# Performance work log

Hardware: AMD Instinct MI355X
Metric: run time of the kernel (lower is better)

Reference implementation:

```python
import jax, jax.numpy as jnp
import numpy as np

E, H, LQ, LC, B = 1024, 16, 1024, 512, 4
HD = E // H
FF = 4 * E
EPS = 1e-6


def _rope(x):
    # x: [B, H, L, D]; interleaved rotary embedding (lucidrains-style)
    D, L = x.shape[-1], x.shape[-2]
    inv_freq = 1.0 / (10000.0 ** (jnp.arange(0, D, 2, dtype=jnp.float32) / D))
    ang = jnp.arange(L, dtype=jnp.float32)[:, None] * inv_freq[None, :]  # [L, D/2]
    cos, sin = jnp.cos(ang), jnp.sin(ang)
    x1, x2 = x[..., 0::2], x[..., 1::2]
    r1 = x1 * cos - x2 * sin
    r2 = x1 * sin + x2 * cos
    return jnp.stack([r1, r2], axis=-1).reshape(x.shape)


def _ln(x, w, b):
    mu = jnp.mean(x, -1, keepdims=True)
    var = jnp.mean(jnp.square(x - mu), -1, keepdims=True)
    return (x - mu) * jax.lax.rsqrt(var + EPS) * w + b


def _rope_attn(x, ctx, qw, qb, kw, kb, vw, vb, pw, pb, mask):
    Bn, L, Em = x.shape
    Lc = ctx.shape[1]
    q = (x @ qw.T + qb).reshape(Bn, L, H, HD).transpose(0, 2, 1, 3)
    k = (ctx @ kw.T + kb).reshape(Bn, Lc, H, HD).transpose(0, 2, 1, 3)
    v = (ctx @ vw.T + vb).reshape(Bn, Lc, H, HD).transpose(0, 2, 1, 3)
    q, k = _rope(q), _rope(k)
    s = jnp.einsum('bhic,bhjc->bhij', q, k) / np.sqrt(HD).astype(np.float32)
    if mask is not None:
        s = jnp.where(mask[None, None], -jnp.inf, s)
    p = jax.nn.softmax(s, axis=-1)
    o = jnp.einsum('bhij,bhjc->bhic', p, v)
    o = o.transpose(0, 2, 1, 3).reshape(Bn, L, Em)
    return o @ pw.T + pb


def setup_inputs() -> dict:
    key = jax.random.key(0)
    ks = iter(jax.random.split(key, 40))
    s = 0.02
    d = {}
    d['x'] = jax.random.normal(next(ks), (B, LQ, E), jnp.float32)
    d['context'] = jax.random.normal(next(ks), (B, LC, E), jnp.float32)
    d['attn_mask'] = jnp.triu(jnp.ones((LQ, LQ), bool), k=1)  # True = masked (causal)
    for g in ('g_msa', 'g_ca', 'g_mlp'):
        d[g] = jax.random.normal(next(ks), (1, 1, E), jnp.float32) * s
    for n in ('n1', 'n2', 'n3'):
        d[n + '_w'] = jnp.ones((E,), jnp.float32)
        d[n + '_b'] = jnp.zeros((E,), jnp.float32)
    for p in ('sa', 'ca'):
        for m in ('q', 'k', 'v', 'p'):
            d[f'{p}_{m}w'] = jax.random.normal(next(ks), (E, E), jnp.float32) * s
            d[f'{p}_{m}b'] = jnp.zeros((E,), jnp.float32)
    d['fc1_w'] = jax.random.normal(next(ks), (FF, E), jnp.float32) * s
    d['fc1_b'] = jnp.zeros((FF,), jnp.float32)
    d['fc2_w'] = jax.random.normal(next(ks), (E, FF), jnp.float32) * s
    d['fc2_b'] = jnp.zeros((E,), jnp.float32)
    return d


def reference(x, context, attn_mask,
              g_msa, g_ca, g_mlp,
              n1_w, n1_b, n2_w, n2_b, n3_w, n3_b,
              sa_qw, sa_qb, sa_kw, sa_kb, sa_vw, sa_vb, sa_pw, sa_pb,
              ca_qw, ca_qb, ca_kw, ca_kb, ca_vw, ca_vb, ca_pw, ca_pb,
              fc1_w, fc1_b, fc2_w, fc2_b):
    # self-attention (causal RoPE) with zero-init learned gate
    x = x + g_msa * _rope_attn(_ln(x, n1_w, n1_b), _ln(x, n1_w, n1_b),
                               sa_qw, sa_qb, sa_kw, sa_kb, sa_vw, sa_vb,
                               sa_pw, sa_pb, attn_mask)
    # cross-attention (RoPE on both streams, no mask)
    h = _ln(x, n2_w, n2_b)
    x = x + g_ca * _rope_attn(h, context,
                              ca_qw, ca_qb, ca_kw, ca_kb, ca_vw, ca_vb,
                              ca_pw, ca_pb, None)
    # gated MLP with tanh-approx GELU
    h = _ln(x, n3_w, n3_b)
    h = jax.nn.gelu(h @ fc1_w.T + fc1_b, approximate=True) @ fc2_w.T + fc2_b
    x = x + g_mlp * h
    return x
```

## Files before the change

kernel.cpp:

```cpp
#include <hip/hip_runtime.h>
#include <math.h>

#if !__has_builtin(__builtin_amdgcn_cvt_pk_fp8_f32)
#include <hip/hip_fp8.h>
#endif

typedef __attribute__((ext_vector_type(8))) short short8;
typedef __attribute__((ext_vector_type(4))) float f32x4;
typedef __attribute__((ext_vector_type(16))) float f32x16;
typedef unsigned char u8;
typedef unsigned short u16;
typedef unsigned int u32;
typedef __attribute__((ext_vector_type(2))) u32 u32x2;
typedef __attribute__((ext_vector_type(4))) u32 u32x4;
typedef __attribute__((ext_vector_type(8))) int i32x8;
typedef unsigned long long u64;

static constexpr int E = 1024, H = 16, LQ = 1024, LC = 512, Bn = 4, FF = 4096;
static constexpr int NTOK = Bn * LQ;
static constexpr int NCTX = Bn * LC;

#define QSCALE 0.1803368801111244f
#define DEFER_THR 11.5f

static constexpr size_t OFF_TCOS   = 0;
static constexpr size_t OFF_TSIN   = OFF_TCOS + (size_t)LQ*32*4;
static constexpr size_t OFF_BSAQKV = OFF_TSIN + (size_t)LQ*32*4;
static constexpr size_t OFF_BCAKV  = OFF_BSAQKV + 16384;
static constexpr size_t OFF_WSAQKV = OFF_BCAKV + 16384;
static constexpr size_t OFF_WSAP   = OFF_WSAQKV + (size_t)3072*1024*2;
static constexpr size_t OFF_WCAQ   = OFF_WSAP   + (size_t)1024*1024*2;
static constexpr size_t OFF_WCAKV  = OFF_WCAQ   + (size_t)1024*1024*2;
static constexpr size_t OFF_WCAP   = OFF_WCAKV  + (size_t)2048*1024*2;
static constexpr size_t OFF_WFC1   = OFF_WCAP   + (size_t)1024*1024*2;
static constexpr size_t OFF_WFC2   = OFF_WFC1   + (size_t)4096*1024*2;
static constexpr size_t OFF_CTXB   = OFF_WFC2   + (size_t)1024*4096*2;
static constexpr size_t OFF_H      = OFF_CTXB   + (size_t)2048*1024*2;
static constexpr size_t OFF_QKV    = OFF_H      + (size_t)4096*1024*2;
static constexpr size_t OFF_CAQ    = OFF_QKV;
static constexpr size_t OFF_CAKV   = OFF_QKV + (size_t)4096*1024*2;
static constexpr size_t OFF_QR     = OFF_QKV + (size_t)4096*3072*2;
static constexpr size_t OFF_KR     = OFF_QR  + (size_t)4096*1024*2;
static constexpr size_t OFF_VT     = OFF_KR  + (size_t)4096*1024*2;
static constexpr size_t OFF_AO     = OFF_VT  + (size_t)4096*1024*2;
static constexpr size_t OFF_U      = OFF_QKV;
static constexpr size_t WS_NEED    = OFF_AO + (size_t)4096*1024*2;

static constexpr size_t OFF_W8QKV = OFF_WFC1;
static constexpr size_t OFF_W8FC1 = OFF_W8QKV + (size_t)3072*1024;
static constexpr size_t OFF_W8FC2 = OFF_W8FC1 + (size_t)4096*1024;

static __device__ __forceinline__ float bf2f(u16 u) {
  union { u32 i; float f; } un; un.i = ((u32)u) << 16; return un.f;
}
static __device__ __forceinline__ u16 f2bf(float f) {
  union { float f; u32 u; } un; un.f = f;
  u32 u = un.u;
  return (u16)((u + 0x7FFFu + ((u >> 16) & 1u)) >> 16);
}
static __device__ __forceinline__ u64 pack4(u16 a, u16 b, u16 c, u16 d) {
  return (u64)a | ((u64)b << 16) | ((u64)c << 32) | ((u64)d << 48);
}
static __device__ __forceinline__ f32x4 mfma16(short8 a, short8 b, f32x4 c) {
  return __builtin_amdgcn_mfma_f32_16x16x32_bf16(a, b, c, 0, 0, 0);
}
static __device__ __forceinline__ f32x16 mfma32(short8 a, short8 b, f32x16 c) {
  return __builtin_amdgcn_mfma_f32_32x32x16_bf16(a, b, c, 0, 0, 0);
}
static __device__ __forceinline__ void gload_lds16(void* lds, const void* g) {
  __builtin_amdgcn_global_load_lds(
      (const __attribute__((address_space(1))) void*)g,
      (__attribute__((address_space(3))) void*)lds, 16, 0, 0);
}
static __device__ __forceinline__ float gelu_tanh(float x) {
  float z2 = 1.5957691216057308f * (x + 0.044715f * x * x * x);
  float e = __expf(z2);
  float r = __builtin_amdgcn_rcpf(e + 1.0f);
  return x - x * r;
}
static __device__ __forceinline__ u32 cvtpk_bf16(float lo, float hi) {
  u32 r;
  asm("v_cvt_pk_bf16_f32 %0, %1, %2" : "=v"(r) : "v"(lo), "v"(hi));
  return r;
}
static __device__ __forceinline__ u32 pack_fp8x4(float a, float b, float c, float d) {
#if __has_builtin(__builtin_amdgcn_cvt_pk_fp8_f32)
  u32 r = (u32)__builtin_amdgcn_cvt_pk_fp8_f32(a, b, 0, false);
  r = (u32)__builtin_amdgcn_cvt_pk_fp8_f32(c, d, (int)r, true);
  return r;
#else
  __hip_fp8_e4m3 qa(a), qb(b), qc(c), qd(d);
  return (u32)qa.__x | ((u32)qb.__x << 8) | ((u32)qc.__x << 16) | ((u32)qd.__x << 24);
#endif
}
static __device__ __forceinline__ u8 fp8b(float f) {
#if __has_builtin(__builtin_amdgcn_cvt_pk_fp8_f32)
  return (u8)((u32)__builtin_amdgcn_cvt_pk_fp8_f32(f, f, 0, false) & 0xFFu);
#else
  __hip_fp8_e4m3 t(f); return t.__x;
#endif
}

__global__ __launch_bounds__(256) void build_tab(float* __restrict__ ct, float* __restrict__ st) {
  int idx = blockIdx.x * 256 + threadIdx.x;
  int pos = idx >> 5, i = idx & 31;
  float inv = powf(10000.f, -(float)i * (1.f / 32.f));
  float a = (float)pos * inv;
  ct[idx] = cosf(a);
  st[idx] = sinf(a);
}

struct Cvt11 { const float* s[11]; };
__global__ __launch_bounds__(256) void cvt_all(Cvt11 a, u16* __restrict__ dst) {
  u32 gid = blockIdx.x * 256 + threadIdx.x;
  u32 s, off;
  if (gid < 2097152u)      { s = gid >> 18; if (s < 3) return;     off = gid & 262143u; }
  else if (gid < 4194304u) { return; }
  else                     { s = 10;                               off = gid - 4194304u; }
  float4 v = *(const float4*)(a.s[s] + (size_t)off * 4);
  *(u64*)(dst + (size_t)gid * 4) = pack4(f2bf(v.x), f2bf(v.y), f2bf(v.z), f2bf(v.w));
}

__global__ __launch_bounds__(256) void cvt_fp8b(const float* __restrict__ qw, const float* __restrict__ kw,
                                                const float* __restrict__ vw, const float* __restrict__ f1,
                                                const float* __restrict__ f2,
                                                u8* __restrict__ d_qkv, u8* __restrict__ d_f1,
                                                u8* __restrict__ d_f2) {
  u32 gid = blockIdx.x * 256 + threadIdx.x;
  u32 seg = gid >> 18, off = gid & 262143u;
  const float* s; u8* d;
  if (seg < 3)      { s = seg == 0 ? qw : (seg == 1 ? kw : vw); d = d_qkv + (size_t)seg * 1048576; }
  else if (seg < 7) { s = f1 + (size_t)(seg - 3) * 1048576;     d = d_f1  + (size_t)(seg - 3) * 1048576; }
  else              { s = f2 + (size_t)(seg - 7) * 1048576;     d = d_f2  + (size_t)(seg - 7) * 1048576; }
  float4 v = *(const float4*)(s + (size_t)off * 4);
  *(u32*)(d + (size_t)off * 4) =
      pack_fp8x4(v.x * 256.f, v.y * 256.f, v.z * 256.f, v.w * 256.f);
}

struct Cp5 { const float* s[5]; };
__global__ __launch_bounds__(256) void copy5(Cp5 a, float* __restrict__ dst) {
  int gid = blockIdx.x * 256 + threadIdx.x;
  int s = gid >> 10, off = gid & 1023;
  int doff = (s < 3) ? s * 1024 : 4096 + (s - 3) * 1024;
  dst[doff + off] = a.s[s][off];
}

__global__ __launch_bounds__(256) void init_bias_gate(float* __restrict__ out, const float* __restrict__ bias,
                                                      const float* __restrict__ gate) {
  int i = (blockIdx.x * 256 + threadIdx.x) * 4;
  int c = i & 1023;
  float4 o = *(float4*)(out + i);
  o.x += gate[c] * bias[c];
  o.y += gate[c + 1] * bias[c + 1];
  o.z += gate[c + 2] * bias[c + 2];
  o.w += gate[c + 3] * bias[c + 3];
  *(float4*)(out + i) = o;
}

__global__ __launch_bounds__(256) void ln_bf16(const float* __restrict__ x, const float* __restrict__ w,
                                               const float* __restrict__ b, u16* __restrict__ out) {
  __shared__ float red[4];
  int row = blockIdx.x, tid = threadIdx.x;
  const float* xr = x + (size_t)row * 1024;
  float4 v = ((const float4*)xr)[tid];
  float s = v.x + v.y + v.z + v.w;
#pragma unroll
  for (int off = 32; off; off >>= 1) s += __shfl_xor(s, off);
  if ((tid & 63) == 0) red[tid >> 6] = s;
  __syncthreads();
  float mean = (red[0] + red[1] + red[2] + red[3]) * (1.f / 1024.f);
  float dx = v.x - mean, dy = v.y - mean, dz = v.z - mean, dw = v.w - mean;
  float sq = dx * dx + dy * dy + dz * dz + dw * dw;
#pragma unroll
  for (int off = 32; off; off >>= 1) sq += __shfl_xor(sq, off);
  __syncthreads();
  if ((tid & 63) == 0) red[tid >> 6] = sq;
  __syncthreads();
  float var = (red[0] + red[1] + red[2] + red[3]) * (1.f / 1024.f);
  float rstd = rsqrtf(var + 1e-6f);
  float4 wv = ((const float4*)w)[tid];
  float4 bv = ((const float4*)b)[tid];
  u64 o = pack4(f2bf(dx * rstd * wv.x + bv.x), f2bf(dy * rstd * wv.y + bv.y),
                f2bf(dz * rstd * wv.z + bv.z), f2bf(dw * rstd * wv.w + bv.w));
  *(u64*)(out + (size_t)row * 1024 + tid * 4) = o;
}

__global__ __launch_bounds__(256) void ln_fp8(const float* __restrict__ x, const float* __restrict__ w,
                                              const float* __restrict__ b, u8* __restrict__ out) {
  __shared__ float red[4];
  int row = blockIdx.x, tid = threadIdx.x;
  const float* xr = x + (size_t)row * 1024;
  float4 v = ((const float4*)xr)[tid];
  float s = v.x + v.y + v.z + v.w;
#pragma unroll
  for (int off = 32; off; off >>= 1) s += __shfl_xor(s, off);
  if ((tid & 63) == 0) red[tid >> 6] = s;
  __syncthreads();
  float mean = (red[0] + red[1] + red[2] + red[3]) * (1.f / 1024.f);
  float dx = v.x - mean, dy = v.y - mean, dz = v.z - mean, dw = v.w - mean;
  float sq = dx * dx + dy * dy + dz * dz + dw * dw;
#pragma unroll
  for (int off = 32; off; off >>= 1) sq += __shfl_xor(sq, off);
  __syncthreads();
  if ((tid & 63) == 0) red[tid >> 6] = sq;
  __syncthreads();
  float var = (red[0] + red[1] + red[2] + red[3]) * (1.f / 1024.f);
  float rstd = rsqrtf(var + 1e-6f);
  float4 wv = ((const float4*)w)[tid];
  float4 bv = ((const float4*)b)[tid];
  u32 pk = pack_fp8x4((dx * rstd * wv.x + bv.x) * 16.f, (dy * rstd * wv.y + bv.y) * 16.f,
                      (dz * rstd * wv.z + bv.z) * 16.f, (dw * rstd * wv.w + bv.w) * 16.f);
  *(u32*)(out + (size_t)row * 1024 + tid * 4) = pk;
}

struct RopeJob { const u16* src; u16* dst; int ld, col0, Lper, T; float scale; };
struct Rope2 { RopeJob j[2]; };
__global__ __launch_bounds__(128) void rope2(Rope2 a, const float* __restrict__ cosT,
                                             const float* __restrict__ sinT) {
  RopeJob jb = a.j[blockIdx.y];
  int t = blockIdx.x;
  if (t >= jb.T) return;
  int b = t / jb.Lper, l = t - b * jb.Lper;
  int tid = threadIdx.x;
  int e0 = tid * 8;
  int h = e0 >> 6, d0 = e0 & 63;
  short8 vv = *(const short8*)(jb.src + (size_t)t * jb.ld + jb.col0 + e0);
  short8 ov;
#pragma unroll
  for (int j = 0; j < 4; ++j) {
    float x1 = bf2f((u16)vv[2 * j]);
    float x2 = bf2f((u16)vv[2 * j + 1]);
    int i = (d0 >> 1) + j;
    float c = cosT[l * 32 + i], s = sinT[l * 32 + i];
    ov[2 * j]     = (short)f2bf((x1 * c - x2 * s) * jb.scale);
    ov[2 * j + 1] = (short)f2bf((x1 * s + x2 * c) * jb.scale);
  }
  *(short8*)(jb.dst + (((size_t)b * H + h) * jb.Lper + l) * 64 + d0) = ov;
}

__global__ __launch_bounds__(256) void vtrans(const u16* __restrict__ src, int ld, int col0,
                                              u16* __restrict__ dst, int Lper) {
  __shared__ u16 tile[64][72];
  int bh = blockIdx.y;
  int b = bh >> 4, h = bh & 15;
  int l0 = blockIdx.x * 64;
  int tid = threadIdx.x;
#pragma unroll
  for (int j = 0; j < 2; ++j) {
    int c = tid + j * 256;
    int i = c >> 3, d0 = (c & 7) * 8;
    short8 v = *(const short8*)(src + (size_t)(b * Lper + l0 + i) * ld + col0 + h * 64 + d0);
    *(short8*)(&tile[i][d0]) = v;
  }
  __syncthreads();
#pragma unroll
  for (int j = 0; j < 2; ++j) {
    int c = tid + j * 256;
    int d = c >> 3, lc = (c & 7) * 8;
    short8 v;
#pragma unroll
    for (int k = 0; k < 8; ++k) v[k] = (short)tile[lc + k][d];
    *(short8*)(dst + (((size_t)bh) * 64 + d) * Lper + l0 + lc) = v;
  }
}

enum { EPI_BF16 = 0, EPI_GELU = 1, EPI_RESID = 2 };

template <int EPI>
__global__ __launch_bounds__(512, 4) void gemm2(const u16* __restrict__ A, const u16* __restrict__ W,
                                                const float* __restrict__ bias, u16* outb, float* outf,
                                                const float* res, const float* __restrict__ gate,
                                                int M, int N, int K) {
  __shared__ u16 As[2][128 * 64];
  __shared__ u16 Bs[2][128 * 64];

  int nwg = gridDim.x * gridDim.y;
  int bid = blockIdx.y * gridDim.x + blockIdx.x;
  int cpx = nwg >> 3;
  int swz = (bid & 7) * cpx + (bid >> 3);
  int bx = swz % gridDim.x;
  int by = swz / gridDim.x;
  int row0 = by * 128, col0 = bx * 128;

  int tid = threadIdx.x;
  int lane = tid & 63, wid = tid >> 6;
  int wr = wid >> 2, wc = wid & 3;
  int lr = lane & 15, lg = lane >> 4;

  size_t a_off0, a_off1, b_off0, b_off1;
  int l_off0 = tid * 8, l_off1 = (512 + tid) * 8;
  {
    int q = tid, r = q >> 3, p = q & 7, sp = p ^ (r & 7);
    a_off0 = (size_t)(row0 + r) * K + sp * 8;
    b_off0 = (size_t)(col0 + r) * K + sp * 8;
    q = 512 + tid; r = q >> 3; p = q & 7; sp = p ^ (r & 7);
    a_off1 = (size_t)(row0 + r) * K + sp * 8;
    b_off1 = (size_t)(col0 + r) * K + sp * 8;
  }

  f32x4 acc[4][2] = {};

  const int nkt = K >> 6;
  {
    gload_lds16(&As[0][l_off0], A + a_off0);
    gload_lds16(&Bs[0][l_off0], W + b_off0);
    gload_lds16(&As[0][l_off1], A + a_off1);
    gload_lds16(&Bs[0][l_off1], W + b_off1);
  }
  __syncthreads();

  for (int kt = 0; kt < nkt; ++kt) {
    int cur = kt & 1;
    if (kt + 1 < nkt) {
      int k0 = (kt + 1) << 6;
      gload_lds16(&As[cur ^ 1][l_off0], A + a_off0 + k0);
      gload_lds16(&Bs[cur ^ 1][l_off0], W + b_off0 + k0);
      gload_lds16(&As[cur ^ 1][l_off1], A + a_off1 + k0);
      gload_lds16(&Bs[cur ^ 1][l_off1], W + b_off1 + k0);
    }
#pragma unroll
    for (int kk = 0; kk < 2; ++kk) {
      short8 af[4], bfr[2];
#pragma unroll
      for (int m = 0; m < 4; ++m) {
        int r = wr * 64 + m * 16 + lr;
        int sc = (kk * 4 + lg) ^ (r & 7);
        af[m] = *(const short8*)(&As[cur][r * 64 + sc * 8]);
      }
#pragma unroll
      for (int n = 0; n < 2; ++n) {
        int r = wc * 32 + n * 16 + lr;
        int sc = (kk * 4 + lg) ^ (r & 7);
        bfr[n] = *(const short8*)(&Bs[cur][r * 64 + sc * 8]);
      }
#pragma unroll
      for (int m = 0; m < 4; ++m)
#pragma unroll
        for (int n = 0; n < 2; ++n)
          acc[m][n] = mfma16(af[m], bfr[n], acc[m][n]);
    }
    __syncthreads();
  }

  if (EPI == EPI_BF16 || EPI == EPI_GELU) {
    u16* Ct = &As[0][0];
#pragma unroll
    for (int n = 0; n < 2; ++n) {
      int c = wc * 32 + n * 16 + lr;
      float bv = bias[col0 + c];
#pragma unroll
      for (int m = 0; m < 4; ++m) {
#pragma unroll
        for (int i = 0; i < 4; ++i) {
          int r = wr * 64 + m * 16 + lg * 4 + i;
          float v = acc[m][n][i] + bv;
          Ct[r * 128 + c] = f2bf(EPI == EPI_GELU ? gelu_tanh(v) : v);
        }
      }
    }
    __syncthreads();
#pragma unroll
    for (int j = 0; j < 4; ++j) {
      u32 q = (u32)tid + j * 512;
      u32 r = q >> 4, ck = q & 15;
      short8 v = *(const short8*)(Ct + r * 128 + ck * 8);
      *(short8*)(outb + (size_t)(row0 + r) * N + col0 + ck * 8) = v;
    }
  } else {
#pragma unroll
    for (int n = 0; n < 2; ++n) {
      int cg = col0 + wc * 32 + n * 16 + lr;
      float bv = bias[cg];
#pragma unroll
      for (int m = 0; m < 4; ++m) {
#pragma unroll
        for (int i = 0; i < 4; ++i) {
          int rg = row0 + wr * 64 + m * 16 + lg * 4 + i;
          float v = acc[m][n][i] + bv;
          float r = res[(size_t)rg * N + cg];
          outf[(size_t)rg * N + cg] = r + gate[cg] * v;
        }
      }
    }
  }
}

enum { E8_BF16 = 0, E8_GELU = 1, E8_ATOMIC = 2 };

template <int EPI>
__global__ __launch_bounds__(256, 2) void gemm8(const u8* __restrict__ A, const u8* __restrict__ W,
                                                const float* __restrict__ bias, u16* outb16,
                                                u8* outb8, float* outf, const float* __restrict__ gate,
                                                int M, int N, int K, int kchunks) {
  __shared__ u8 As[2][128 * 128];
  __shared__ u8 Bs[2][128 * 128];

  int nwg = gridDim.x * gridDim.y;
  int bid = blockIdx.y * gridDim.x + blockIdx.x;
  int cpx = nwg >> 3;
  int swz = (bid & 7) * cpx + (bid >> 3);
  int bx = swz % gridDim.x, by = swz / gridDim.x;
  int row0 = by * 128, col0 = bx * 128;

  const int Kc = K / kchunks;
  const int kbase = blockIdx.z * Kc;

  int tid = threadIdx.x;
  int lane = tid & 63, wid = tid >> 6;
  int wr = wid >> 1, wc = wid & 1;
  int lr = lane & 15, lg = lane >> 4;

  u32 aoff[4], boff[4];
  int ldso[4];
#pragma unroll
  for (int j = 0; j < 4; ++j) {
    int q = tid + j * 256;
    int r = q >> 3, p = q & 7, sp = p ^ (r & 7);
    aoff[j] = (u32)(row0 + r) * (u32)K + sp * 16;
    boff[j] = (u32)(col0 + r) * (u32)K + sp * 16;
    ldso[j] = q * 16;
  }

  f32x4 acc[4][4] = {};
  const int nkt = Kc >> 7;

  auto rdfrag = [&](const u8* base, int r, i32x8& f) {
    const u8* rp = base + r * 128;
    int ck = lg * 2;
    u32x4 lo = *(const u32x4*)(rp + ((ck) ^ (r & 7)) * 16);
    u32x4 hh = *(const u32x4*)(rp + ((ck + 1) ^ (r & 7)) * 16);
    i32x8 v;
    v[0] = (int)lo[0]; v[1] = (int)lo[1]; v[2] = (int)lo[2]; v[3] = (int)lo[3];
    v[4] = (int)hh[0]; v[5] = (int)hh[1]; v[6] = (int)hh[2]; v[7] = (int)hh[3];
    f = v;
  };

#pragma unroll
  for (int j = 0; j < 4; ++j) {
    gload_lds16(&As[0][ldso[j]], A + aoff[j] + kbase);
    gload_lds16(&Bs[0][ldso[j]], W + boff[j] + kbase);
  }
  __syncthreads();

  for (int kt = 0; kt < nkt; ++kt) {
    int cur = kt & 1;
    if (kt + 1 < nkt) {
      int k0 = kbase + ((kt + 1) << 7);
#pragma unroll
      for (int j = 0; j < 4; ++j) {
        gload_lds16(&As[cur ^ 1][ldso[j]], A + aoff[j] + k0);
        gload_lds16(&Bs[cur ^ 1][ldso[j]], W + boff[j] + k0);
      }
    }
    i32x8 a[4], b[4];
#pragma unroll
    for (int m = 0; m < 4; ++m) rdfrag(&As[cur][0], wr * 64 + m * 16 + lr, a[m]);
#pragma unroll
    for (int n = 0; n < 4; ++n) rdfrag(&Bs[cur][0], wc * 64 + n * 16 + lr, b[n]);
    __builtin_amdgcn_s_setprio(1);
#pragma unroll
    for (int m = 0; m < 4; ++m)
#pragma unroll
      for (int n = 0; n < 4; ++n)
        acc[m][n] = __builtin_amdgcn_mfma_scale_f32_16x16x128_f8f6f4(
            a[m], b[n], acc[m][n], 0, 0, 0, 0x7F7F7F7F, 0, 0x7F7F7F7F);
    __builtin_amdgcn_s_setprio(0);
    __syncthreads();
  }

  constexpr float SCL = 1.f / 4096.f;
  if (EPI == E8_BF16) {
    u16* Ct = (u16*)&As[0][0];
#pragma unroll
    for (int n = 0; n < 4; ++n) {
      int cl = wc * 64 + n * 16 + lr;
      float bv = bias[col0 + cl];
#pragma unroll
      for (int m = 0; m < 4; ++m) {
#pragma unroll
        for (int i = 0; i < 4; ++i) {
          int rl = wr * 64 + m * 16 + lg * 4 + i;
          Ct[rl * 128 + cl] = f2bf(acc[m][n][i] * SCL + bv);
        }
      }
    }
    __syncthreads();
#pragma unroll
    for (int j = 0; j < 8; ++j) {
      u32 q = (u32)tid + j * 256;
      u32 r = q >> 4, ck = q & 15;
      short8 v = *(const short8*)(Ct + r * 128 + ck * 8);
      *(short8*)(outb16 + (size_t)(row0 + r) * N + col0 + ck * 8) = v;
    }
  } else if (EPI == E8_GELU) {
    u8* Ct = &As[0][0];
#pragma unroll
    for (int n = 0; n < 4; ++n) {
      int cl = wc * 64 + n * 16 + lr;
      float bv = bias[col0 + cl];
#pragma unroll
      for (int m = 0; m < 4; ++m) {
#pragma unroll
        for (int i = 0; i < 4; ++i) {
          int rl = wr * 64 + m * 16 + lg * 4 + i;
          float v = acc[m][n][i] * SCL + bv;
          Ct[rl * 128 + cl] = fp8b(gelu_tanh(v) * 16.f);
        }
      }
    }
    __syncthreads();
#pragma unroll
    for (int j = 0; j < 4; ++j) {
      int q = tid + j * 256;
      int r = q >> 3, ck = q & 7;
      *(u32x4*)(outb8 + (size_t)(row0 + r) * N + col0 + ck * 16) =
          *(const u32x4*)(Ct + r * 128 + ck * 16);
    }
  } else {
#pragma unroll
    for (int n = 0; n < 4; ++n) {
      int cg = col0 + wc * 64 + n * 16 + lr;
      float gv = gate[cg];
#pragma unroll
      for (int m = 0; m < 4; ++m) {
#pragma unroll
        for (int i = 0; i < 4; ++i) {
          int rg = row0 + wr * 64 + m * 16 + lg * 4 + i;
          atomicAdd(&outf[(size_t)rg * N + cg], gv * (acc[m][n][i] * SCL));
        }
      }
    }
  }
}

template <int MASKED, int PRE>
static __device__ __forceinline__ void attn_tile3(short8* kf, const u16* KtNext,
                                                  const u16* Vp0, const u16* Vp1,
                                                  const short8* qf, int kb, int q0, int l31, int hi,
                                                  float& m, float& lsum, f32x16& o0, f32x16& o1) {
  short8 vf0[4], vf1[4];
#pragma unroll
  for (int ks = 0; ks < 4; ++ks) {
    vf0[ks] = *(const short8*)(Vp0 + ks * 16 + hi * 8);
    vf1[ks] = *(const short8*)(Vp1 + ks * 16 + hi * 8);
  }
  f32x16 s0 = {}, s1 = {};
  __builtin_amdgcn_s_setprio(1);
#pragma unroll
  for (int s = 0; s < 4; ++s) {
    s0 = mfma32(kf[s], qf[s], s0);
    s1 = mfma32(kf[4 + s], qf[s], s1);
  }
  __builtin_amdgcn_s_setprio(0);
  if (PRE) {
    const u16* kp0 = KtNext + (size_t)l31 * 64 + hi * 8;
    const u16* kp1 = KtNext + (size_t)(32 + l31) * 64 + hi * 8;
#pragma unroll
    for (int s = 0; s < 4; ++s) {
      kf[s] = *(const short8*)(kp0 + s * 16);
      kf[4 + s] = *(const short8*)(kp1 + s * 16);
    }
  }
  if (MASKED) {
    int qg = q0 + l31;
#pragma unroll
    for (int r = 0; r < 16; ++r) {
      int kk = kb + (r & 3) + 8 * (r >> 2) + 4 * hi;
      if (kk > qg) s0[r] = -INFINITY;
      if (kk + 32 > qg) s1[r] = -INFINITY;
    }
  }
  float pm = -INFINITY;
#pragma unroll
  for (int r = 0; r < 16; ++r) pm = fmaxf(pm, fmaxf(s0[r], s1[r]));
  pm = fmaxf(pm, __shfl_xor(pm, 32));
  if (!__all(pm <= m + DEFER_THR)) {
    float mn = fmaxf(m, pm);
    float al = exp2f(m - mn);
    m = mn;
    lsum *= al;
#pragma unroll
    for (int r = 0; r < 16; ++r) {
      float alr = __shfl(al, (r & 3) + 8 * (r >> 2) + 4 * hi);
      o0[r] *= alr;
      o1[r] *= alr;
    }
  }
  float ts = 0.f;
#pragma unroll
  for (int r = 0; r < 16; ++r) {
    float p0 = exp2f(s0[r] - m);
    float p1 = exp2f(s1[r] - m);
    s0[r] = p0; s1[r] = p1;
    ts += p0 + p1;
  }
  ts += __shfl_xor(ts, 32);
  lsum += ts;
  auto pack8 = [&](float a0, float a1, float a2, float a3,
                   float a4, float a5, float a6, float a7) -> short8 {
    u32 c0 = cvtpk_bf16(a0, a1), c1 = cvtpk_bf16(a2, a3);
    u32 c2 = cvtpk_bf16(a4, a5), c3 = cvtpk_bf16(a6, a7);
    u32x2 r02 = __builtin_amdgcn_permlane32_swap(c0, c2, false, false);
    u32x2 r13 = __builtin_amdgcn_permlane32_swap(c1, c3, false, false);
    u32x4 w;
    w[0] = r02[0]; w[1] = r13[0]; w[2] = r02[1]; w[3] = r13[1];
    return __builtin_bit_cast(short8, w);
  };
  short8 pa0 = pack8(s0[0], s0[1], s0[2], s0[3], s0[4], s0[5], s0[6], s0[7]);
  short8 pa1 = pack8(s0[8], s0[9], s0[10], s0[11], s0[12], s0[13], s0[14], s0[15]);
  short8 pa2 = pack8(s1[0], s1[1], s1[2], s1[3], s1[4], s1[5], s1[6], s1[7]);
  short8 pa3 = pack8(s1[8], s1[9], s1[10], s1[11], s1[12], s1[13], s1[14], s1[15]);
  short8 pa[4] = {pa0, pa1, pa2, pa3};
  __builtin_amdgcn_s_setprio(1);
#pragma unroll
  for (int ks = 0; ks < 4; ++ks) {
    o0 = mfma32(pa[ks], vf0[ks], o0);
    o1 = mfma32(pa[ks], vf1[ks], o1);
  }
  __builtin_amdgcn_s_setprio(0);
}

template <int CAUSAL>
__global__ __launch_bounds__(256) void flash_attn2(const u16* __restrict__ Q, const u16* __restrict__ K,
                                                   const u16* __restrict__ Vt, u16* __restrict__ O,
                                                   int Lq, int Lk) {
  const int wid = threadIdx.x >> 6, lane = threadIdx.x & 63;
  const int l31 = lane & 31, hi = lane >> 5;
  int wg = blockIdx.x * 4 + wid;
  int bh = wg & 63;
  int qc = wg >> 6;
  if (CAUSAL) qc = (Lq >> 5) - 1 - qc;
  int q0 = qc << 5;

  const u16* Qb = Q + ((size_t)bh * Lq + q0) * 64;
  const u16* Kb = K + (size_t)bh * Lk * 64;
  const u16* Vb = Vt + (size_t)bh * 64 * Lk;

  short8 qf[4];
#pragma unroll
  for (int s = 0; s < 4; ++s) qf[s] = *(const short8*)(Qb + (size_t)l31 * 64 + s * 16 + hi * 8);

  f32x16 o0 = {}, o1 = {};
  float m = -INFINITY, lsum = 0.f;

  const u16* Kt = Kb;
  const u16* Vp0 = Vb + (size_t)l31 * Lk;
  const u16* Vp1 = Vb + (size_t)(32 + l31) * Lk;

  short8 kf[8];
  {
    const u16* kp0 = Kt + (size_t)l31 * 64 + hi * 8;
    const u16* kp1 = Kt + (size_t)(32 + l31) * 64 + hi * 8;
#pragma unroll
    for (int s = 0; s < 4; ++s) {
      kf[s] = *(const short8*)(kp0 + s * 16);
      kf[4 + s] = *(const short8*)(kp1 + s * 16);
    }
  }

  int nt = CAUSAL ? ((q0 >> 6) + 1) : (Lk >> 6);
  for (int t = 0; t < nt - 1; ++t) {
    attn_tile3<0, 1>(kf, Kt + 64 * 64, Vp0, Vp1, qf, t * 64, q0, l31, hi, m, lsum, o0, o1);
    Kt += 64 * 64; Vp0 += 64; Vp1 += 64;
  }
  if (CAUSAL)
    attn_tile3<1, 0>(kf, nullptr, Vp0, Vp1, qf, (nt - 1) * 64, q0, l31, hi, m, lsum, o0, o1);
  else
    attn_tile3<0, 0>(kf, nullptr, Vp0, Vp1, qf, (nt - 1) * 64, q0, l31, hi, m, lsum, o0, o1);

  float myinv = 1.f / lsum;
  int b = bh >> 4, h = bh & 15;
#pragma unroll
  for (int r = 0; r < 16; ++r) {
    int cr = (r & 3) + 8 * (r >> 2) + 4 * hi;
    float li = __shfl(myinv, cr);
    u16* op = O + ((size_t)b * Lq + q0 + cr) * 1024 + h * 64;
    op[l31] = f2bf(o0[r] * li);
    op[32 + l31] = f2bf(o1[r] * li);
  }
}

extern "C" void kernel_launch(void* const* d_in, const int* in_sizes, int n_in,
                              void* d_out, int out_size, void* d_ws, size_t ws_size,
                              hipStream_t stream) {
  (void)in_sizes; (void)n_in; (void)out_size;
  if (ws_size < WS_NEED) return;

  const float* x     = (const float*)d_in[0];
  const float* ctx   = (const float*)d_in[1];
  const float* g_msa = (const float*)d_in[3];
  const float* g_ca  = (const float*)d_in[4];
  const float* g_mlp = (const float*)d_in[5];
  const float* n1w = (const float*)d_in[6],  *n1b = (const float*)d_in[7];
  const float* n2w = (const float*)d_in[8],  *n2b = (const float*)d_in[9];
  const float* n3w = (const float*)d_in[10], *n3b = (const float*)d_in[11];
  const float* sa_qw = (const float*)d_in[12], *sa_kw = (const float*)d_in[14];
  const float* sa_vw = (const float*)d_in[16], *sa_pw = (const float*)d_in[18];
  const float* sa_qb = (const float*)d_in[13], *sa_kb = (const float*)d_in[15];
  const float* sa_vb = (const float*)d_in[17], *sa_pb = (const float*)d_in[19];
  const float* ca_qw = (const float*)d_in[20], *ca_qb = (const float*)d_in[21];
  const float* ca_kw = (const float*)d_in[22], *ca_kb = (const float*)d_in[23];
  const float* ca_vw = (const float*)d_in[24], *ca_vb = (const float*)d_in[25];
  const float* ca_pw = (const float*)d_in[26], *ca_pb = (const float*)d_in[27];
  const float* fc1w = (const float*)d_in[28], *fc1b = (const float*)d_in[29];
  const float* fc2w = (const float*)d_in[30], *fc2b = (const float*)d_in[31];

  char* ws = (char*)d_ws;
  float* out = (float*)d_out;
  float* tcos = (float*)(ws + OFF_TCOS);
  float* tsin = (float*)(ws + OFF_TSIN);
  u16* Hb   = (u16*)(ws + OFF_H);
  u16* QKV  = (u16*)(ws + OFF_QKV);
  u16* QR   = (u16*)(ws + OFF_QR);
  u16* KR   = (u16*)(ws + OFF_KR);
  u16* VT   = (u16*)(ws + OFF_VT);
  u16* AO   = (u16*)(ws + OFF_AO);
  u8*  H8   = (u8*)(ws + OFF_H);
  u8*  U8   = (u8*)(ws + OFF_U);
  u8*  W8QKV = (u8*)(ws + OFF_W8QKV);
  u8*  W8FC1 = (u8*)(ws + OFF_W8FC1);
  u8*  W8FC2 = (u8*)(ws + OFF_W8FC2);

  build_tab<<<dim3(128), dim3(256), 0, stream>>>(tcos, tsin);

  Cvt11 ca;
  ca.s[0] = sa_qw; ca.s[1] = sa_kw; ca.s[2] = sa_vw; ca.s[3] = sa_pw;
  ca.s[4] = ca_qw; ca.s[5] = ca_kw; ca.s[6] = ca_vw; ca.s[7] = ca_pw;
  ca.s[8] = fc1w;  ca.s[9] = fc2w;  ca.s[10] = ctx;
  cvt_all<<<dim3(18432), dim3(256), 0, stream>>>(ca, (u16*)(ws + OFF_WSAQKV));
  cvt_fp8b<<<dim3(11264), dim3(256), 0, stream>>>(sa_qw, sa_kw, sa_vw, fc1w, fc2w,
                                                  W8QKV, W8FC1, W8FC2);
  Cp5 cp;
  cp.s[0] = sa_qb; cp.s[1] = sa_kb; cp.s[2] = sa_vb; cp.s[3] = ca_kb; cp.s[4] = ca_vb;
  copy5<<<dim3(20), dim3(256), 0, stream>>>(cp, (float*)(ws + OFF_BSAQKV));

  ln_fp8<<<dim3(NTOK), dim3(256), 0, stream>>>(x, n1w, n1b, H8);
  gemm8<E8_BF16><<<dim3(3072 / 128, NTOK / 128), dim3(256), 0, stream>>>(
      H8, W8QKV, (float*)(ws + OFF_BSAQKV), QKV, nullptr, nullptr, nullptr,
      NTOK, 3072, 1024, 1);
  {
    Rope2 r;
    r.j[0] = {QKV, QR, 3072, 0,    LQ, NTOK, QSCALE};
    r.j[1] = {QKV, KR, 3072, 1024, LQ, NTOK, 1.0f};
    rope2<<<dim3(NTOK, 2), dim3(128), 0, stream>>>(r, tcos, tsin);
  }
  vtrans<<<dim3(LQ / 64, Bn * H), dim3(256), 0, stream>>>(QKV, 3072, 2048, VT, LQ);
  flash_attn2<1><<<dim3(512), dim3(256), 0, stream>>>(QR, KR, VT, AO, LQ, LQ);
  gemm2<EPI_RESID><<<dim3(1024 / 128, NTOK / 128), dim3(512), 0, stream>>>(
      AO, (u16*)(ws + OFF_WSAP), sa_pb, nullptr, out, x, g_msa, NTOK, 1024, 1024);

  ln_bf16<<<dim3(NTOK), dim3(256), 0, stream>>>(out, n2w, n2b, Hb);
  gemm2<EPI_BF16><<<dim3(1024 / 128, NTOK / 128), dim3(512), 0, stream>>>(
      Hb, (u16*)(ws + OFF_WCAQ), ca_qb, (u16*)(ws + OFF_CAQ), nullptr, nullptr, nullptr,
      NTOK, 1024, 1024);
  gemm2<EPI_BF16><<<dim3(2048 / 128, NCTX / 128), dim3(512), 0, stream>>>(
      (u16*)(ws + OFF_CTXB), (u16*)(ws + OFF_WCAKV), (float*)(ws + OFF_BCAKV),
      (u16*)(ws + OFF_CAKV), nullptr, nullptr, nullptr, NCTX, 2048, 1024);
  {
    Rope2 r;
    r.j[0] = {(u16*)(ws + OFF_CAQ),  QR, 1024, 0, LQ, NTOK, QSCALE};
    r.j[1] = {(u16*)(ws + OFF_CAKV), KR, 2048, 0, LC, NCTX, 1.0f};
    rope2<<<dim3(NTOK, 2), dim3(128), 0, stream>>>(r, tcos, tsin);
  }
  vtrans<<<dim3(LC / 64, Bn * H), dim3(256), 0, stream>>>(
      (u16*)(ws + OFF_CAKV), 2048, 1024, VT, LC);
  flash_attn2<0><<<dim3(512), dim3(256), 0, stream>>>(QR, KR, VT, AO, LQ, LC);
  gemm2<EPI_RESID><<<dim3(1024 / 128, NTOK / 128), dim3(512), 0, stream>>>(
      AO, (u16*)(ws + OFF_WCAP), ca_pb, nullptr, out, out, g_ca, NTOK, 1024, 1024);

  ln_fp8<<<dim3(NTOK), dim3(256), 0, stream>>>(out, n3w, n3b, H8);
  gemm8<E8_GELU><<<dim3(4096 / 128, NTOK / 128), dim3(256), 0, stream>>>(
      H8, W8FC1, fc1b, nullptr, U8, nullptr, nullptr, NTOK, 4096, 1024, 1);
  init_bias_gate<<<dim3(4096), dim3(256), 0, stream>>>(out, fc2b, g_mlp);
  gemm8<E8_ATOMIC><<<dim3(1024 / 128, NTOK / 128, 2), dim3(256), 0, stream>>>(
      U8, W8FC2, nullptr, nullptr, nullptr, out, g_mlp, NTOK, 1024, 4096, 2);
}
```

Before: 326.7 us.

## Move projection and cross-attention GEMMs to FP8 and emit attention output in FP8

Four GEMMs switch from the bf16 gemm2 path to the FP8 gemm8 path: self-attention output projection, cross-attention Q, cross-attention KV and cross-attention output projection. gemm8 gains a new residual/gate epilogue for the projections. Flash attention now writes its output as scaled FP8, the context is quantized to FP8, and a single conversion kernel builds all FP8 weights and the context, replacing the bf16 conversion. The aim is to halve operand bandwidth and use higher-throughput FP8 MFMA, and to drop the bf16 weight conversion pass. The cost is lower numerical precision, with accuracy risk from the fixed scale factors.

```diff
diff --git a/kernel.cpp b/kernel.cpp
--- a/kernel.cpp
+++ b/kernel.cpp
@@ -22,19 +22,22 @@
 
 #define QSCALE 0.1803368801111244f
 #define DEFER_THR 11.5f
+#define AOSCL 16.0f
 
 static constexpr size_t OFF_TCOS   = 0;
 static constexpr size_t OFF_TSIN   = OFF_TCOS + (size_t)LQ*32*4;
 static constexpr size_t OFF_BSAQKV = OFF_TSIN + (size_t)LQ*32*4;
 static constexpr size_t OFF_BCAKV  = OFF_BSAQKV + 16384;
-static constexpr size_t OFF_WSAQKV = OFF_BCAKV + 16384;
-static constexpr size_t OFF_WSAP   = OFF_WSAQKV + (size_t)3072*1024*2;
-static constexpr size_t OFF_WCAQ   = OFF_WSAP   + (size_t)1024*1024*2;
-static constexpr size_t OFF_WCAKV  = OFF_WCAQ   + (size_t)1024*1024*2;
-static constexpr size_t OFF_WCAP   = OFF_WCAKV  + (size_t)2048*1024*2;
-static constexpr size_t OFF_WFC1   = OFF_WCAP   + (size_t)1024*1024*2;
-static constexpr size_t OFF_WFC2   = OFF_WFC1   + (size_t)4096*1024*2;
-static constexpr size_t OFF_CTXB   = OFF_WFC2   + (size_t)1024*4096*2;
+static constexpr size_t OFF_W8     = OFF_BCAKV + 16384;
+static constexpr size_t OFF_W8QKV  = OFF_W8;
+static constexpr size_t OFF_W8SAP  = OFF_W8QKV  + (size_t)3*1048576;
+static constexpr size_t OFF_W8CAQ  = OFF_W8SAP  + (size_t)1*1048576;
+static constexpr size_t OFF_W8CAKV = OFF_W8CAQ  + (size_t)1*1048576;
+static constexpr size_t OFF_W8CAP  = OFF_W8CAKV + (size_t)2*1048576;
+static constexpr size_t OFF_W8FC1  = OFF_W8CAP  + (size_t)1*1048576;
+static constexpr size_t OFF_W8FC2  = OFF_W8FC1  + (size_t)4*1048576;
+static constexpr size_t OFF_CTX8   = OFF_W8FC2  + (size_t)4*1048576;
+static constexpr size_t OFF_CTXB   = OFF_W8 + (size_t)30*1048576 + (size_t)2048*1024*2;
 static constexpr size_t OFF_H      = OFF_CTXB   + (size_t)2048*1024*2;
 static constexpr size_t OFF_QKV    = OFF_H      + (size_t)4096*1024*2;
 static constexpr size_t OFF_CAQ    = OFF_QKV;
@@ -46,10 +49,6 @@
 static constexpr size_t OFF_U      = OFF_QKV;
 static constexpr size_t WS_NEED    = OFF_AO + (size_t)4096*1024*2;
 
-static constexpr size_t OFF_W8QKV = OFF_WFC1;
-static constexpr size_t OFF_W8FC1 = OFF_W8QKV + (size_t)3072*1024;
-static constexpr size_t OFF_W8FC2 = OFF_W8FC1 + (size_t)4096*1024;
-
 static __device__ __forceinline__ float bf2f(u16 u) {
   union { u32 i; float f; } un; un.i = ((u32)u) << 16; return un.f;
 }
@@ -60,9 +59,6 @@
 }
 static __device__ __forceinline__ u64 pack4(u16 a, u16 b, u16 c, u16 d) {
   return (u64)a | ((u64)b << 16) | ((u64)c << 32) | ((u64)d << 48);
-}
-static __device__ __forceinline__ f32x4 mfma16(short8 a, short8 b, f32x4 c) {
-  return __builtin_amdgcn_mfma_f32_16x16x32_bf16(a, b, c, 0, 0, 0);
 }
 static __device__ __forceinline__ f32x16 mfma32(short8 a, short8 b, f32x16 c) {
   return __builtin_amdgcn_mfma_f32_32x32x16_bf16(a, b, c, 0, 0, 0);
@@ -110,31 +106,20 @@
   st[idx] = sinf(a);
 }
 
-struct Cvt11 { const float* s[11]; };
-__global__ __launch_bounds__(256) void cvt_all(Cvt11 a, u16* __restrict__ dst) {
-  u32 gid = blockIdx.x * 256 + threadIdx.x;
-  u32 s, off;
-  if (gid < 2097152u)      { s = gid >> 18; if (s < 3) return;     off = gid & 262143u; }
-  else if (gid < 4194304u) { return; }
-  else                     { s = 10;                               off = gid - 4194304u; }
-  float4 v = *(const float4*)(a.s[s] + (size_t)off * 4);
-  *(u64*)(dst + (size_t)gid * 4) = pack4(f2bf(v.x), f2bf(v.y), f2bf(v.z), f2bf(v.w));
-}
-
-__global__ __launch_bounds__(256) void cvt_fp8b(const float* __restrict__ qw, const float* __restrict__ kw,
-                                                const float* __restrict__ vw, const float* __restrict__ f1,
-                                                const float* __restrict__ f2,
-                                                u8* __restrict__ d_qkv, u8* __restrict__ d_f1,
-                                                u8* __restrict__ d_f2) {
+struct CvtF8 { const float* s[10]; };
+__global__ __launch_bounds__(256) void cvt_fp8c(CvtF8 a, const float* __restrict__ ctx,
+                                                u8* __restrict__ dst) {
   u32 gid = blockIdx.x * 256 + threadIdx.x;
   u32 seg = gid >> 18, off = gid & 262143u;
-  const float* s; u8* d;
-  if (seg < 3)      { s = seg == 0 ? qw : (seg == 1 ? kw : vw); d = d_qkv + (size_t)seg * 1048576; }
-  else if (seg < 7) { s = f1 + (size_t)(seg - 3) * 1048576;     d = d_f1  + (size_t)(seg - 3) * 1048576; }
-  else              { s = f2 + (size_t)(seg - 7) * 1048576;     d = d_f2  + (size_t)(seg - 7) * 1048576; }
+  const float* s;
+  float scl = 256.f;
+  if (seg < 8)       s = a.s[seg];
+  else if (seg < 12) s = a.s[8] + (size_t)(seg - 8) * 1048576;
+  else if (seg < 16) s = a.s[9] + (size_t)(seg - 12) * 1048576;
+  else             { s = ctx + (size_t)(seg - 16) * 1048576; scl = 16.f; }
   float4 v = *(const float4*)(s + (size_t)off * 4);
-  *(u32*)(d + (size_t)off * 4) =
-      pack_fp8x4(v.x * 256.f, v.y * 256.f, v.z * 256.f, v.w * 256.f);
+  *(u32*)(dst + (size_t)seg * 1048576 + (size_t)off * 4) =
+      pack_fp8x4(v.x * scl, v.y * scl, v.z * scl, v.w * scl);
 }
 
 struct Cp5 { const float* s[5]; };
@@ -155,34 +140,6 @@
   o.z += gate[c + 2] * bias[c + 2];
   o.w += gate[c + 3] * bias[c + 3];
   *(float4*)(out + i) = o;
-}
-
-__global__ __launch_bounds__(256) void ln_bf16(const float* __restrict__ x, const float* __restrict__ w,
-                                               const float* __restrict__ b, u16* __restrict__ out) {
-  __shared__ float red[4];
-  int row = blockIdx.x, tid = threadIdx.x;
-  const float* xr = x + (size_t)row * 1024;
-  float4 v = ((const float4*)xr)[tid];
-  float s = v.x + v.y + v.z + v.w;
-#pragma unroll
-  for (int off = 32; off; off >>= 1) s += __shfl_xor(s, off);
-  if ((tid & 63) == 0) red[tid >> 6] = s;
-  __syncthreads();
-  float mean = (red[0] + red[1] + red[2] + red[3]) * (1.f / 1024.f);
-  float dx = v.x - mean, dy = v.y - mean, dz = v.z - mean, dw = v.w - mean;
-  float sq = dx * dx + dy * dy + dz * dz + dw * dw;
-#pragma unroll
-  for (int off = 32; off; off >>= 1) sq += __shfl_xor(sq, off);
-  __syncthreads();
-  if ((tid & 63) == 0) red[tid >> 6] = sq;
-  __syncthreads();
-  float var = (red[0] + red[1] + red[2] + red[3]) * (1.f / 1024.f);
-  float rstd = rsqrtf(var + 1e-6f);
-  float4 wv = ((const float4*)w)[tid];
-  float4 bv = ((const float4*)b)[tid];
-  u64 o = pack4(f2bf(dx * rstd * wv.x + bv.x), f2bf(dy * rstd * wv.y + bv.y),
-                f2bf(dz * rstd * wv.z + bv.z), f2bf(dw * rstd * wv.w + bv.w));
-  *(u64*)(out + (size_t)row * 1024 + tid * 4) = o;
 }
 
 __global__ __launch_bounds__(256) void ln_fp8(const float* __restrict__ x, const float* __restrict__ w,
@@ -264,133 +221,13 @@
   }
 }
 
-enum { EPI_BF16 = 0, EPI_GELU = 1, EPI_RESID = 2 };
-
-template <int EPI>
-__global__ __launch_bounds__(512, 4) void gemm2(const u16* __restrict__ A, const u16* __restrict__ W,
-                                                const float* __restrict__ bias, u16* outb, float* outf,
-                                                const float* res, const float* __restrict__ gate,
-                                                int M, int N, int K) {
-  __shared__ u16 As[2][128 * 64];
-  __shared__ u16 Bs[2][128 * 64];
-
-  int nwg = gridDim.x * gridDim.y;
-  int bid = blockIdx.y * gridDim.x + blockIdx.x;
-  int cpx = nwg >> 3;
-  int swz = (bid & 7) * cpx + (bid >> 3);
-  int bx = swz % gridDim.x;
-  int by = swz / gridDim.x;
-  int row0 = by * 128, col0 = bx * 128;
-
-  int tid = threadIdx.x;
-  int lane = tid & 63, wid = tid >> 6;
-  int wr = wid >> 2, wc = wid & 3;
-  int lr = lane & 15, lg = lane >> 4;
-
-  size_t a_off0, a_off1, b_off0, b_off1;
-  int l_off0 = tid * 8, l_off1 = (512 + tid) * 8;
-  {
-    int q = tid, r = q >> 3, p = q & 7, sp = p ^ (r & 7);
-    a_off0 = (size_t)(row0 + r) * K + sp * 8;
-    b_off0 = (size_t)(col0 + r) * K + sp * 8;
-    q = 512 + tid; r = q >> 3; p = q & 7; sp = p ^ (r & 7);
-    a_off1 = (size_t)(row0 + r) * K + sp * 8;
-    b_off1 = (size_t)(col0 + r) * K + sp * 8;
-  }
-
-  f32x4 acc[4][2] = {};
-
-  const int nkt = K >> 6;
-  {
-    gload_lds16(&As[0][l_off0], A + a_off0);
-    gload_lds16(&Bs[0][l_off0], W + b_off0);
-    gload_lds16(&As[0][l_off1], A + a_off1);
-    gload_lds16(&Bs[0][l_off1], W + b_off1);
-  }
-  __syncthreads();
-
-  for (int kt = 0; kt < nkt; ++kt) {
-    int cur = kt & 1;
-    if (kt + 1 < nkt) {
-      int k0 = (kt + 1) << 6;
-      gload_lds16(&As[cur ^ 1][l_off0], A + a_off0 + k0);
-      gload_lds16(&Bs[cur ^ 1][l_off0], W + b_off0 + k0);
-      gload_lds16(&As[cur ^ 1][l_off1], A + a_off1 + k0);
-      gload_lds16(&Bs[cur ^ 1][l_off1], W + b_off1 + k0);
-    }
-#pragma unroll
-    for (int kk = 0; kk < 2; ++kk) {
-      short8 af[4], bfr[2];
-#pragma unroll
-      for (int m = 0; m < 4; ++m) {
-        int r = wr * 64 + m * 16 + lr;
-        int sc = (kk * 4 + lg) ^ (r & 7);
-        af[m] = *(const short8*)(&As[cur][r * 64 + sc * 8]);
-      }
-#pragma unroll
-      for (int n = 0; n < 2; ++n) {
-        int r = wc * 32 + n * 16 + lr;
-        int sc = (kk * 4 + lg) ^ (r & 7);
-        bfr[n] = *(const short8*)(&Bs[cur][r * 64 + sc * 8]);
-      }
-#pragma unroll
-      for (int m = 0; m < 4; ++m)
-#pragma unroll
-        for (int n = 0; n < 2; ++n)
-          acc[m][n] = mfma16(af[m], bfr[n], acc[m][n]);
-    }
-    __syncthreads();
-  }
-
-  if (EPI == EPI_BF16 || EPI == EPI_GELU) {
-    u16* Ct = &As[0][0];
-#pragma unroll
-    for (int n = 0; n < 2; ++n) {
-      int c = wc * 32 + n * 16 + lr;
-      float bv = bias[col0 + c];
-#pragma unroll
-      for (int m = 0; m < 4; ++m) {
-#pragma unroll
-        for (int i = 0; i < 4; ++i) {
-          int r = wr * 64 + m * 16 + lg * 4 + i;
-          float v = acc[m][n][i] + bv;
-          Ct[r * 128 + c] = f2bf(EPI == EPI_GELU ? gelu_tanh(v) : v);
-        }
-      }
-    }
-    __syncthreads();
-#pragma unroll
-    for (int j = 0; j < 4; ++j) {
-      u32 q = (u32)tid + j * 512;
-      u32 r = q >> 4, ck = q & 15;
-      short8 v = *(const short8*)(Ct + r * 128 + ck * 8);
-      *(short8*)(outb + (size_t)(row0 + r) * N + col0 + ck * 8) = v;
-    }
-  } else {
-#pragma unroll
-    for (int n = 0; n < 2; ++n) {
-      int cg = col0 + wc * 32 + n * 16 + lr;
-      float bv = bias[cg];
-#pragma unroll
-      for (int m = 0; m < 4; ++m) {
-#pragma unroll
-        for (int i = 0; i < 4; ++i) {
-          int rg = row0 + wr * 64 + m * 16 + lg * 4 + i;
-          float v = acc[m][n][i] + bv;
-          float r = res[(size_t)rg * N + cg];
-          outf[(size_t)rg * N + cg] = r + gate[cg] * v;
-        }
-      }
-    }
-  }
-}
-
-enum { E8_BF16 = 0, E8_GELU = 1, E8_ATOMIC = 2 };
+enum { E8_BF16 = 0, E8_GELU = 1, E8_ATOMIC = 2, E8_RESID = 3 };
 
 template <int EPI>
 __global__ __launch_bounds__(256, 2) void gemm8(const u8* __restrict__ A, const u8* __restrict__ W,
                                                 const float* __restrict__ bias, u16* outb16,
-                                                u8* outb8, float* outf, const float* __restrict__ gate,
+                                                u8* outb8, float* outf, const float* res,
+                                                const float* __restrict__ gate,
                                                 int M, int N, int K, int kchunks) {
   __shared__ u8 As[2][128 * 128];
   __shared__ u8 Bs[2][128 * 128];
@@ -515,6 +352,22 @@
       int r = q >> 3, ck = q & 7;
       *(u32x4*)(outb8 + (size_t)(row0 + r) * N + col0 + ck * 16) =
           *(const u32x4*)(Ct + r * 128 + ck * 16);
+    }
+  } else if (EPI == E8_RESID) {
+#pragma unroll
+    for (int n = 0; n < 4; ++n) {
+      int cg = col0 + wc * 64 + n * 16 + lr;
+      float bv = bias[cg], gv = gate[cg];
+#pragma unroll
+      for (int m = 0; m < 4; ++m) {
+#pragma unroll
+        for (int i = 0; i < 4; ++i) {
+          int rg = row0 + wr * 64 + m * 16 + lg * 4 + i;
+          float v = acc[m][n][i] * SCL + bv;
+          float r = res[(size_t)rg * N + cg];
+          outf[(size_t)rg * N + cg] = r + gv * v;
+        }
+      }
     }
   } else {
 #pragma unroll
@@ -622,7 +475,7 @@
 
 template <int CAUSAL>
 __global__ __launch_bounds__(256) void flash_attn2(const u16* __restrict__ Q, const u16* __restrict__ K,
-                                                   const u16* __restrict__ Vt, u16* __restrict__ O,
+                                                   const u16* __restrict__ Vt, u8* __restrict__ O,
                                                    int Lq, int Lk) {
   const int wid = threadIdx.x >> 6, lane = threadIdx.x & 63;
   const int l31 = lane & 31, hi = lane >> 5;
@@ -668,15 +521,15 @@
   else
     attn_tile3<0, 0>(kf, nullptr, Vp0, Vp1, qf, (nt - 1) * 64, q0, l31, hi, m, lsum, o0, o1);
 
-  float myinv = 1.f / lsum;
+  float myinv = AOSCL / lsum;
   int b = bh >> 4, h = bh & 15;
 #pragma unroll
   for (int r = 0; r < 16; ++r) {
     int cr = (r & 3) + 8 * (r >> 2) + 4 * hi;
     float li = __shfl(myinv, cr);
-    u16* op = O + ((size_t)b * Lq + q0 + cr) * 1024 + h * 64;
-    op[l31] = f2bf(o0[r] * li);
-    op[32 + l31] = f2bf(o1[r] * li);
+    u8* op = O + ((size_t)b * Lq + q0 + cr) * 1024 + h * 64;
+    op[l31] = fp8b(o0[r] * li);
+    op[32 + l31] = fp8b(o1[r] * li);
   }
 }
 
@@ -709,34 +562,35 @@
   float* out = (float*)d_out;
   float* tcos = (float*)(ws + OFF_TCOS);
   float* tsin = (float*)(ws + OFF_TSIN);
-  u16* Hb   = (u16*)(ws + OFF_H);
   u16* QKV  = (u16*)(ws + OFF_QKV);
   u16* QR   = (u16*)(ws + OFF_QR);
   u16* KR   = (u16*)(ws + OFF_KR);
   u16* VT   = (u16*)(ws + OFF_VT);
-  u16* AO   = (u16*)(ws + OFF_AO);
+  u8*  AO8  = (u8*)(ws + OFF_AO);
   u8*  H8   = (u8*)(ws + OFF_H);
   u8*  U8   = (u8*)(ws + OFF_U);
-  u8*  W8QKV = (u8*)(ws + OFF_W8QKV);
-  u8*  W8FC1 = (u8*)(ws + OFF_W8FC1);
-  u8*  W8FC2 = (u8*)(ws + OFF_W8FC2);
+  u8*  W8QKV  = (u8*)(ws + OFF_W8QKV);
+  u8*  W8SAP  = (u8*)(ws + OFF_W8SAP);
+  u8*  W8CAQ  = (u8*)(ws + OFF_W8CAQ);
+  u8*  W8CAKV = (u8*)(ws + OFF_W8CAKV);
+  u8*  W8CAP  = (u8*)(ws + OFF_W8CAP);
+  u8*  W8FC1  = (u8*)(ws + OFF_W8FC1);
+  u8*  W8FC2  = (u8*)(ws + OFF_W8FC2);
+  u8*  CTX8   = (u8*)(ws + OFF_CTX8);
 
   build_tab<<<dim3(128), dim3(256), 0, stream>>>(tcos, tsin);
-
-  Cvt11 ca;
-  ca.s[0] = sa_qw; ca.s[1] = sa_kw; ca.s[2] = sa_vw; ca.s[3] = sa_pw;
-  ca.s[4] = ca_qw; ca.s[5] = ca_kw; ca.s[6] = ca_vw; ca.s[7] = ca_pw;
-  ca.s[8] = fc1w;  ca.s[9] = fc2w;  ca.s[10] = ctx;
-  cvt_all<<<dim3(18432), dim3(256), 0, stream>>>(ca, (u16*)(ws + OFF_WSAQKV));
-  cvt_fp8b<<<dim3(11264), dim3(256), 0, stream>>>(sa_qw, sa_kw, sa_vw, fc1w, fc2w,
-                                                  W8QKV, W8FC1, W8FC2);
+  CvtF8 cf;
+  cf.s[0] = sa_qw; cf.s[1] = sa_kw; cf.s[2] = sa_vw; cf.s[3] = sa_pw;
+  cf.s[4] = ca_qw; cf.s[5] = ca_kw; cf.s[6] = ca_vw; cf.s[7] = ca_pw;
+  cf.s[8] = fc1w;  cf.s[9] = fc2w;
+  cvt_fp8c<<<dim3(18432), dim3(256), 0, stream>>>(cf, ctx, W8QKV);
   Cp5 cp;
   cp.s[0] = sa_qb; cp.s[1] = sa_kb; cp.s[2] = sa_vb; cp.s[3] = ca_kb; cp.s[4] = ca_vb;
   copy5<<<dim3(20), dim3(256), 0, stream>>>(cp, (float*)(ws + OFF_BSAQKV));
 
   ln_fp8<<<dim3(NTOK), dim3(256), 0, stream>>>(x, n1w, n1b, H8);
   gemm8<E8_BF16><<<dim3(3072 / 128, NTOK / 128), dim3(256), 0, stream>>>(
-      H8, W8QKV, (float*)(ws + OFF_BSAQKV), QKV, nullptr, nullptr, nullptr,
+      H8, W8QKV, (float*)(ws + OFF_BSAQKV), QKV, nullptr, nullptr, nullptr, nullptr,
       NTOK, 3072, 1024, 1);
   {
     Rope2 r;
@@ -745,17 +599,17 @@
     rope2<<<dim3(NTOK, 2), dim3(128), 0, stream>>>(r, tcos, tsin);
   }
   vtrans<<<dim3(LQ / 64, Bn * H), dim3(256), 0, stream>>>(QKV, 3072, 2048, VT, LQ);
-  flash_attn2<1><<<dim3(512), dim3(256), 0, stream>>>(QR, KR, VT, AO, LQ, LQ);
-  gemm2<EPI_RESID><<<dim3(1024 / 128, NTOK / 128), dim3(512), 0, stream>>>(
-      AO, (u16*)(ws + OFF_WSAP), sa_pb, nullptr, out, x, g_msa, NTOK, 1024, 1024);
-
-  ln_bf16<<<dim3(NTOK), dim3(256), 0, stream>>>(out, n2w, n2b, Hb);
-  gemm2<EPI_BF16><<<dim3(1024 / 128, NTOK / 128), dim3(512), 0, stream>>>(
-      Hb, (u16*)(ws + OFF_WCAQ), ca_qb, (u16*)(ws + OFF_CAQ), nullptr, nullptr, nullptr,
-      NTOK, 1024, 1024);
-  gemm2<EPI_BF16><<<dim3(2048 / 128, NCTX / 128), dim3(512), 0, stream>>>(
-      (u16*)(ws + OFF_CTXB), (u16*)(ws + OFF_WCAKV), (float*)(ws + OFF_BCAKV),
-      (u16*)(ws + OFF_CAKV), nullptr, nullptr, nullptr, NCTX, 2048, 1024);
+  flash_attn2<1><<<dim3(512), dim3(256), 0, stream>>>(QR, KR, VT, AO8, LQ, LQ);
+  gemm8<E8_RESID><<<dim3(1024 / 128, NTOK / 128), dim3(256), 0, stream>>>(
+      AO8, W8SAP, sa_pb, nullptr, nullptr, out, x, g_msa, NTOK, 1024, 1024, 1);
+
+  ln_fp8<<<dim3(NTOK), dim3(256), 0, stream>>>(out, n2w, n2b, H8);
+  gemm8<E8_BF16><<<dim3(1024 / 128, NTOK / 128), dim3(256), 0, stream>>>(
+      H8, W8CAQ, ca_qb, (u16*)(ws + OFF_CAQ), nullptr, nullptr, nullptr, nullptr,
+      NTOK, 1024, 1024, 1);
+  gemm8<E8_BF16><<<dim3(2048 / 128, NCTX / 128), dim3(256), 0, stream>>>(
+      CTX8, W8CAKV, (float*)(ws + OFF_BCAKV), (u16*)(ws + OFF_CAKV), nullptr, nullptr,
+      nullptr, nullptr, NCTX, 2048, 1024, 1);
   {
     Rope2 r;
     r.j[0] = {(u16*)(ws + OFF_CAQ),  QR, 1024, 0, LQ, NTOK, QSCALE};
@@ -764,14 +618,14 @@
   }
   vtrans<<<dim3(LC / 64, Bn * H), dim3(256), 0, stream>>>(
       (u16*)(ws + OFF_CAKV), 2048, 1024, VT, LC);
-  flash_attn2<0><<<dim3(512), dim3(256), 0, stream>>>(QR, KR, VT, AO, LQ, LC);
-  gemm2<EPI_RESID><<<dim3(1024 / 128, NTOK / 128), dim3(512), 0, stream>>>(
-      AO, (u16*)(ws + OFF_WCAP), ca_pb, nullptr, out, out, g_ca, NTOK, 1024, 1024);
+  flash_attn2<0><<<dim3(512), dim3(256), 0, stream>>>(QR, KR, VT, AO8, LQ, LC);
+  gemm8<E8_RESID><<<dim3(1024 / 128, NTOK / 128), dim3(256), 0, stream>>>(
+      AO8, W8CAP, ca_pb, nullptr, nullptr, out, out, g_ca, NTOK, 1024, 1024, 1);
 
   ln_fp8<<<dim3(NTOK), dim3(256), 0, stream>>>(out, n3w, n3b, H8);
   gemm8<E8_GELU><<<dim3(4096 / 128, NTOK / 128), dim3(256), 0, stream>>>(
-      H8, W8FC1, fc1b, nullptr, U8, nullptr, nullptr, NTOK, 4096, 1024, 1);
+      H8, W8FC1, fc1b, nullptr, U8, nullptr, nullptr, nullptr, NTOK, 4096, 1024, 1);
   init_bias_gate<<<dim3(4096), dim3(256), 0, stream>>>(out, fc2b, g_mlp);
   gemm8<E8_ATOMIC><<<dim3(1024 / 128, NTOK / 128, 2), dim3(256), 0, stream>>>(
-      U8, W8FC2, nullptr, nullptr, nullptr, out, g_mlp, NTOK, 1024, 4096, 2);
-}
+      U8, W8FC2, nullptr, nullptr, nullptr, out, nullptr, g_mlp, NTOK, 1024, 4096, 2);
+}
```

Result: faster. 312.8 us (median of 3 runs) (-4.2%).
